# Optimization experiments

Hardware: AMD Instinct MI355X
Metric: run time of the kernel (lower is better)

Reference implementation:

```python
import jax, jax.numpy as jnp
import numpy as np

N = 8192   # nodes
D = 128    # uniform feature dim (arch = [128,128,128])
L = 2      # num_layers = len(arch)-1
EDGE_P = 0.01

def setup_inputs() -> dict:
    key = jax.random.key(0)
    ks = jax.random.split(key, 11)
    features = jax.random.normal(ks[0], (N, D), dtype=jnp.float32)
    # sparse symmetric adjacency with self-loops (diagonal forced True, as in forward)
    a = jax.random.uniform(ks[1], (N, N)) < EDGE_P
    mask = a | a.T | jnp.eye(N, dtype=bool)
    s = 1.0 / np.sqrt(D)
    def w(k):
        return (jax.random.normal(k, (L, D, D), dtype=jnp.float32) * s)
    def b(k):
        return jax.random.normal(k, (L, D), dtype=jnp.float32) * 0.01
    return {
        "features": features, "mask": mask,
        "Wq": w(ks[2]), "bq": b(ks[3]),
        "Wk": w(ks[4]), "bk": b(ks[5]),
        "Wv": w(ks[6]), "bv": b(ks[7]),
        "Wo": w(ks[8]), "bo": b(ks[9]),
    }

def reference(features, mask, Wq, bq, Wk, bk, Wv, bv, Wo, bo):
    h = features
    outputs = [h]
    for l in range(L):
        Q = h @ Wq[l] + bq[l]                      # [N, D]
        K = h @ Wk[l] + bk[l]
        V = h @ Wv[l] + bv[l]
        scores = (Q @ K.T) * (1.0 / jnp.sqrt(jnp.float32(K.shape[1])))  # [N, N]
        scores = jnp.where(mask, scores, -jnp.inf)
        attn = jax.nn.softmax(scores, axis=1)
        h = attn @ V                                # [N, D]
        h = h @ Wo[l] + bo[l]
        outputs.append(h)
    return tuple(outputs)
```

## Files before the change

kernel.cpp:

```cpp
#include <hip/hip_runtime.h>
#include <hip/hip_bf16.h>
#include <hip/hip_fp16.h>
#include <math.h>

#define N 8192
#define D 128
#define CAP 512

typedef _Float16 f16x2 __attribute__((ext_vector_type(2)));
typedef _Float16 f16x4 __attribute__((ext_vector_type(4)));
typedef _Float16 f16x8 __attribute__((ext_vector_type(8)));

__device__ __forceinline__ float dot2(f16x2 a, f16x2 b, float c) {
#if __has_builtin(__builtin_amdgcn_fdot2)
    return __builtin_amdgcn_fdot2(a, b, c, false);
#else
    return c + (float)a[0] * (float)b[0] + (float)a[1] * (float)b[1];
#endif
}

__device__ __forceinline__ float dot8(f16x8 a, f16x8 b, float c) {
    c = dot2(__builtin_shufflevector(a, a, 0, 1), __builtin_shufflevector(b, b, 0, 1), c);
    c = dot2(__builtin_shufflevector(a, a, 2, 3), __builtin_shufflevector(b, b, 2, 3), c);
    c = dot2(__builtin_shufflevector(a, a, 4, 5), __builtin_shufflevector(b, b, 4, 5), c);
    c = dot2(__builtin_shufflevector(a, a, 6, 7), __builtin_shufflevector(b, b, 6, 7), c);
    return c;
}

__global__ __launch_bounds__(256) void build_adj(const int* __restrict__ mask,
                                                 unsigned short* __restrict__ nbr,
                                                 int* __restrict__ deg) {
    const int i = blockIdx.x;
    __shared__ int cnt;
    if (threadIdx.x == 0) cnt = 0;
    __syncthreads();
    const int4* row = (const int4*)(mask + (size_t)i * N);
    for (int c = threadIdx.x; c < N / 4; c += 256) {
        int4 m4 = row[c];
        int base = 4 * c;
        if (m4.x) { int p = atomicAdd(&cnt, 1); if (p < CAP) nbr[(size_t)i * CAP + p] = (unsigned short)(base); }
        if (m4.y) { int p = atomicAdd(&cnt, 1); if (p < CAP) nbr[(size_t)i * CAP + p] = (unsigned short)(base + 1); }
        if (m4.z) { int p = atomicAdd(&cnt, 1); if (p < CAP) nbr[(size_t)i * CAP + p] = (unsigned short)(base + 2); }
        if (m4.w) { int p = atomicAdd(&cnt, 1); if (p < CAP) nbr[(size_t)i * CAP + p] = (unsigned short)(base + 3); }
    }
    __syncthreads();
    if (threadIdx.x == 0) deg[i] = (cnt > CAP) ? CAP : cnt;
}

__global__ __launch_bounds__(256) void qkv_gemm(const float* __restrict__ A,
                                                const float* __restrict__ Wq, const float* __restrict__ bq,
                                                const float* __restrict__ Wk, const float* __restrict__ bk,
                                                const float* __restrict__ Wv, const float* __restrict__ bv,
                                                __half* __restrict__ Qo, __half* __restrict__ Ko,
                                                __half* __restrict__ Vo,
                                                float* __restrict__ copy_out) {
    __shared__ float As[8][D];
    const int tid = threadIdx.x;
    const int r   = tid >> 5;
    const int jg  = tid & 31;
    const int i0  = blockIdx.x * 8;

    const float4 av = ((const float4*)(A + (size_t)i0 * D))[tid];
    ((float4*)&As[0][0])[tid] = av;
    ((float4*)(copy_out + (size_t)i0 * D))[tid] = av;
    __syncthreads();

    const float* Ws[3] = {Wq, Wk, Wv};
    const float* bs[3] = {bq, bk, bv};
    __half* Os[3] = {Qo, Ko, Vo};

    #pragma unroll
    for (int m = 0; m < 3; ++m) {
        float4 acc = *(const float4*)(bs[m] + 4 * jg);
        const float* W = Ws[m];
        #pragma unroll 8
        for (int k4 = 0; k4 < 32; ++k4) {
            const float4 a4 = *(const float4*)&As[r][4 * k4];
            const float* wb = W + (size_t)(4 * k4) * D + 4 * jg;
            const float4 w0 = *(const float4*)(wb);
            const float4 w1 = *(const float4*)(wb + D);
            const float4 w2 = *(const float4*)(wb + 2 * D);
            const float4 w3 = *(const float4*)(wb + 3 * D);
            acc.x += a4.x * w0.x + a4.y * w1.x + a4.z * w2.x + a4.w * w3.x;
            acc.y += a4.x * w0.y + a4.y * w1.y + a4.z * w2.y + a4.w * w3.y;
            acc.z += a4.x * w0.z + a4.y * w1.z + a4.z * w2.z + a4.w * w3.z;
            acc.w += a4.x * w0.w + a4.y * w1.w + a4.z * w2.w + a4.w * w3.w;
        }
        f16x4 h;
        h[0] = (_Float16)acc.x; h[1] = (_Float16)acc.y;
        h[2] = (_Float16)acc.z; h[3] = (_Float16)acc.w;
        *(f16x4*)(Os[m] + (size_t)(i0 + r) * D + 4 * jg) = h;
    }
}

__global__ __launch_bounds__(256) void gemmO_qkv(const float* __restrict__ Aattn,
                                                 const float* __restrict__ Wo, const float* __restrict__ bo,
                                                 float* __restrict__ Hout,
                                                 const float* __restrict__ Wq, const float* __restrict__ bq,
                                                 const float* __restrict__ Wk, const float* __restrict__ bk,
                                                 const float* __restrict__ Wv, const float* __restrict__ bv,
                                                 __half* __restrict__ Qo, __half* __restrict__ Ko,
                                                 __half* __restrict__ Vo) {
    __shared__ float As[8][D];
    __shared__ float Hs[8][D];
    const int tid = threadIdx.x;
    const int r   = tid >> 5;
    const int jg  = tid & 31;
    const int i0  = blockIdx.x * 8;

    ((float4*)&As[0][0])[tid] = ((const float4*)(Aattn + (size_t)i0 * D))[tid];
    __syncthreads();

    {
        float4 acc = *(const float4*)(bo + 4 * jg);
        #pragma unroll 8
        for (int k4 = 0; k4 < 32; ++k4) {
            const float4 a4 = *(const float4*)&As[r][4 * k4];
            const float* wb = Wo + (size_t)(4 * k4) * D + 4 * jg;
            const float4 w0 = *(const float4*)(wb);
            const float4 w1 = *(const float4*)(wb + D);
            const float4 w2 = *(const float4*)(wb + 2 * D);
            const float4 w3 = *(const float4*)(wb + 3 * D);
            acc.x += a4.x * w0.x + a4.y * w1.x + a4.z * w2.x + a4.w * w3.x;
            acc.y += a4.x * w0.y + a4.y * w1.y + a4.z * w2.y + a4.w * w3.y;
            acc.z += a4.x * w0.z + a4.y * w1.z + a4.z * w2.z + a4.w * w3.z;
            acc.w += a4.x * w0.w + a4.y * w1.w + a4.z * w2.w + a4.w * w3.w;
        }
        *(float4*)(Hout + (size_t)(i0 + r) * D + 4 * jg) = acc;
        *(float4*)&Hs[r][4 * jg] = acc;
    }
    __syncthreads();

    const float* Ws[3] = {Wq, Wk, Wv};
    const float* bs[3] = {bq, bk, bv};
    __half* Os[3] = {Qo, Ko, Vo};
    #pragma unroll
    for (int m = 0; m < 3; ++m) {
        float4 acc = *(const float4*)(bs[m] + 4 * jg);
        const float* W = Ws[m];
        #pragma unroll 8
        for (int k4 = 0; k4 < 32; ++k4) {
            const float4 a4 = *(const float4*)&Hs[r][4 * k4];
            const float* wb = W + (size_t)(4 * k4) * D + 4 * jg;
            const float4 w0 = *(const float4*)(wb);
            const float4 w1 = *(const float4*)(wb + D);
            const float4 w2 = *(const float4*)(wb + 2 * D);
            const float4 w3 = *(const float4*)(wb + 3 * D);
            acc.x += a4.x * w0.x + a4.y * w1.x + a4.z * w2.x + a4.w * w3.x;
            acc.y += a4.x * w0.y + a4.y * w1.y + a4.z * w2.y + a4.w * w3.y;
            acc.z += a4.x * w0.z + a4.y * w1.z + a4.z * w2.z + a4.w * w3.z;
            acc.w += a4.x * w0.w + a4.y * w1.w + a4.z * w2.w + a4.w * w3.w;
        }
        f16x4 h;
        h[0] = (_Float16)acc.x; h[1] = (_Float16)acc.y;
        h[2] = (_Float16)acc.z; h[3] = (_Float16)acc.w;
        *(f16x4*)(Os[m] + (size_t)(i0 + r) * D + 4 * jg) = h;
    }
}

__global__ __launch_bounds__(256) void gemm_bias(const float* __restrict__ A,
                                                 const float* __restrict__ W,
                                                 const float* __restrict__ bias,
                                                 float* __restrict__ C) {
    __shared__ float As[8][D];
    const int tid = threadIdx.x;
    const int r   = tid >> 5;
    const int jg  = tid & 31;
    const int i0  = blockIdx.x * 8;

    ((float4*)&As[0][0])[tid] = ((const float4*)(A + (size_t)i0 * D))[tid];
    __syncthreads();

    float4 acc = *(const float4*)(bias + 4 * jg);
    #pragma unroll 8
    for (int k4 = 0; k4 < 32; ++k4) {
        const float4 a4 = *(const float4*)&As[r][4 * k4];
        const float* wb = W + (size_t)(4 * k4) * D + 4 * jg;
        const float4 w0 = *(const float4*)(wb);
        const float4 w1 = *(const float4*)(wb + D);
        const float4 w2 = *(const float4*)(wb + 2 * D);
        const float4 w3 = *(const float4*)(wb + 3 * D);
        acc.x += a4.x * w0.x + a4.y * w1.x + a4.z * w2.x + a4.w * w3.x;
        acc.y += a4.x * w0.y + a4.y * w1.y + a4.z * w2.y + a4.w * w3.y;
        acc.z += a4.x * w0.z + a4.y * w1.z + a4.z * w2.z + a4.w * w3.z;
        acc.w += a4.x * w0.w + a4.y * w1.w + a4.z * w2.w + a4.w * w3.w;
    }
    *(float4*)(C + (size_t)(i0 + r) * D + 4 * jg) = acc;
}

__global__ __launch_bounds__(256) void attn_sparse(const __half* __restrict__ Q,
                                                   const __half* __restrict__ K,
                                                   const __half* __restrict__ V,
                                                   const unsigned short* __restrict__ nbr,
                                                   const int* __restrict__ deg,
                                                   float* __restrict__ Hout) {
    const int i    = blockIdx.x;
    const int tid  = threadIdx.x;
    const int wave = tid >> 6;
    const int lane = tid & 63;
    const int g    = lane >> 4;
    const int gl   = lane & 15;

    __shared__ float          s[CAP];
    __shared__ unsigned short jls[CAP];
    __shared__ float          red[16][D];
    __shared__ float          inv_sh;

    const int dg = min(deg[i], CAP);
    for (int e = tid; e < dg; e += 256) jls[e] = nbr[(size_t)i * CAP + e];
    const f16x8 qv = ((const f16x8*)(Q + (size_t)i * D))[gl];
    __syncthreads();

    const float scale = 0.088388347648318447f;

    for (int e = wave * 4 + g; e < dg; e += 16) {
        const f16x8 kv = ((const f16x8*)(K + (size_t)jls[e] * D))[gl];
        float dot = dot8(kv, qv, 0.f);
        dot += __shfl_xor(dot, 1);
        dot += __shfl_xor(dot, 2);
        dot += __shfl_xor(dot, 4);
        dot += __shfl_xor(dot, 8);
        if (gl == 0) s[e] = __expf(dot * scale);
    }
    __syncthreads();

    if (wave == 0) {
        float ls = 0.f;
        for (int e = lane; e < dg; e += 64) ls += s[e];
        #pragma unroll
        for (int off = 32; off > 0; off >>= 1)
            ls += __shfl_xor(ls, off);
        if (lane == 0) inv_sh = 1.0f / ls;
    }
    __syncthreads();

    const int slice = tid >> 4;
    float acc[8] = {0.f, 0.f, 0.f, 0.f, 0.f, 0.f, 0.f, 0.f};
    for (int e = slice; e < dg; e += 16) {
        const float p  = s[e];
        const f16x8 v8 = ((const f16x8*)(V + (size_t)jls[e] * D))[gl];
        #pragma unroll
        for (int k = 0; k < 8; ++k) acc[k] += p * (float)v8[k];
    }
    #pragma unroll
    for (int k = 0; k < 8; ++k) red[slice][8 * gl + k] = acc[k];
    __syncthreads();
    if (tid < D) {
        float sum = 0.f;
        #pragma unroll
        for (int sl = 0; sl < 16; ++sl) sum += red[sl][tid];
        Hout[(size_t)i * D + tid] = sum * inv_sh;
    }
}

extern "C" void kernel_launch(void* const* d_in, const int* in_sizes, int n_in,
                              void* d_out, int out_size, void* d_ws, size_t ws_size,
                              hipStream_t stream) {
    const float* features = (const float*)d_in[0];
    const int*   mask     = (const int*)d_in[1];
    const float* Wq = (const float*)d_in[2];
    const float* bq = (const float*)d_in[3];
    const float* Wk = (const float*)d_in[4];
    const float* bk = (const float*)d_in[5];
    const float* Wv = (const float*)d_in[6];
    const float* bv = (const float*)d_in[7];
    const float* Wo = (const float*)d_in[8];
    const float* bo = (const float*)d_in[9];
    float* out = (float*)d_out;

    char* base = (char*)d_ws;
    unsigned short* nbr = (unsigned short*)base;
    int*    deg  = (int*)(base + (size_t)N * CAP * 2);
    __half* Qb16 = (__half*)(base + (size_t)N * CAP * 2 + N * 4);
    __half* Kb16 = Qb16 + (size_t)N * D;
    __half* Vb16 = Kb16 + (size_t)N * D;
    float*  tmp  = (float*)(Vb16 + (size_t)N * D);

    build_adj<<<N, 256, 0, stream>>>(mask, nbr, deg);

    qkv_gemm<<<N / 8, 256, 0, stream>>>(features, Wq, bq, Wk, bk, Wv, bv,
                                        Qb16, Kb16, Vb16, out);
    attn_sparse<<<N, 256, 0, stream>>>(Qb16, Kb16, Vb16, nbr, deg, tmp);
    gemmO_qkv<<<N / 8, 256, 0, stream>>>(tmp, Wo, bo, out + (size_t)N * D,
                                         Wq + D * D, bq + D, Wk + D * D, bk + D,
                                         Wv + D * D, bv + D, Qb16, Kb16, Vb16);
    attn_sparse<<<N, 256, 0, stream>>>(Qb16, Kb16, Vb16, nbr, deg, tmp);
    gemm_bias<<<N / 8, 256, 0, stream>>>(tmp, Wo + D * D, bo + D,
                                         out + (size_t)2 * N * D);
}
```

Baseline: 610.3 us.

## Process one node per wave with fused single-pass softmax-weighted aggregation

The sparse attention kernel now assigns one destination node to each wavefront, so each block covers four nodes, instead of using a whole 256-thread block per node. The score, exp, denominator and V-accumulation steps are fused into one loop over neighbours, removing the shared score buffer, the separate reduction pass and two block barriers. Partial sums across the four 16-lane groups are combined with shuffles. It skips max subtraction, as the code before also did, and each wave still handles roughly 160 neighbours serially, so there is less parallelism per node.

```diff
diff --git a/kernel.cpp b/kernel.cpp
--- a/kernel.cpp
+++ b/kernel.cpp
@@ -194,62 +194,57 @@
                                                    const unsigned short* __restrict__ nbr,
                                                    const int* __restrict__ deg,
                                                    float* __restrict__ Hout) {
-    const int i    = blockIdx.x;
     const int tid  = threadIdx.x;
     const int wave = tid >> 6;
     const int lane = tid & 63;
     const int g    = lane >> 4;
     const int gl   = lane & 15;
-
-    __shared__ float          s[CAP];
-    __shared__ unsigned short jls[CAP];
-    __shared__ float          red[16][D];
-    __shared__ float          inv_sh;
+    const int i    = blockIdx.x * 4 + wave;
+
+    __shared__ unsigned short jls[4][CAP];
 
     const int dg = min(deg[i], CAP);
-    for (int e = tid; e < dg; e += 256) jls[e] = nbr[(size_t)i * CAP + e];
+    for (int e = lane; e < dg; e += 64)
+        jls[wave][e] = nbr[(size_t)i * CAP + e];
     const f16x8 qv = ((const f16x8*)(Q + (size_t)i * D))[gl];
     __syncthreads();
 
     const float scale = 0.088388347648318447f;
 
-    for (int e = wave * 4 + g; e < dg; e += 16) {
-        const f16x8 kv = ((const f16x8*)(K + (size_t)jls[e] * D))[gl];
+    float acc[8] = {0.f, 0.f, 0.f, 0.f, 0.f, 0.f, 0.f, 0.f};
+    float denom  = 0.f;
+
+    for (int e = g; e < dg; e += 4) {
+        const int j = jls[wave][e];
+        const f16x8 kv = ((const f16x8*)(K + (size_t)j * D))[gl];
         float dot = dot8(kv, qv, 0.f);
         dot += __shfl_xor(dot, 1);
         dot += __shfl_xor(dot, 2);
         dot += __shfl_xor(dot, 4);
         dot += __shfl_xor(dot, 8);
-        if (gl == 0) s[e] = __expf(dot * scale);
-    }
-    __syncthreads();
-
-    if (wave == 0) {
-        float ls = 0.f;
-        for (int e = lane; e < dg; e += 64) ls += s[e];
-        #pragma unroll
-        for (int off = 32; off > 0; off >>= 1)
-            ls += __shfl_xor(ls, off);
-        if (lane == 0) inv_sh = 1.0f / ls;
-    }
-    __syncthreads();
-
-    const int slice = tid >> 4;
-    float acc[8] = {0.f, 0.f, 0.f, 0.f, 0.f, 0.f, 0.f, 0.f};
-    for (int e = slice; e < dg; e += 16) {
-        const float p  = s[e];
-        const f16x8 v8 = ((const f16x8*)(V + (size_t)jls[e] * D))[gl];
+        const float p = __expf(dot * scale);
+        const f16x8 v8 = ((const f16x8*)(V + (size_t)j * D))[gl];
         #pragma unroll
         for (int k = 0; k < 8; ++k) acc[k] += p * (float)v8[k];
-    }
+        denom += p;
+    }
+
     #pragma unroll
-    for (int k = 0; k < 8; ++k) red[slice][8 * gl + k] = acc[k];
-    __syncthreads();
-    if (tid < D) {
-        float sum = 0.f;
-        #pragma unroll
-        for (int sl = 0; sl < 16; ++sl) sum += red[sl][tid];
-        Hout[(size_t)i * D + tid] = sum * inv_sh;
+    for (int k = 0; k < 8; ++k) {
+        acc[k] += __shfl_xor(acc[k], 16);
+        acc[k] += __shfl_xor(acc[k], 32);
+    }
+    denom += __shfl_xor(denom, 16);
+    denom += __shfl_xor(denom, 32);
+
+    if (g == 0) {
+        const float inv = 1.0f / denom;
+        float4 o0, o1;
+        o0.x = acc[0] * inv; o0.y = acc[1] * inv; o0.z = acc[2] * inv; o0.w = acc[3] * inv;
+        o1.x = acc[4] * inv; o1.y = acc[5] * inv; o1.z = acc[6] * inv; o1.w = acc[7] * inv;
+        float4* dst = (float4*)(Hout + (size_t)i * D + 8 * gl);
+        dst[0] = o0;
+        dst[1] = o1;
     }
 }
 
@@ -280,11 +275,11 @@
 
     qkv_gemm<<<N / 8, 256, 0, stream>>>(features, Wq, bq, Wk, bk, Wv, bv,
                                         Qb16, Kb16, Vb16, out);
-    attn_sparse<<<N, 256, 0, stream>>>(Qb16, Kb16, Vb16, nbr, deg, tmp);
+    attn_sparse<<<N / 4, 256, 0, stream>>>(Qb16, Kb16, Vb16, nbr, deg, tmp);
     gemmO_qkv<<<N / 8, 256, 0, stream>>>(tmp, Wo, bo, out + (size_t)N * D,
                                          Wq + D * D, bq + D, Wk + D * D, bk + D,
                                          Wv + D * D, bv + D, Qb16, Kb16, Vb16);
-    attn_sparse<<<N, 256, 0, stream>>>(Qb16, Kb16, Vb16, nbr, deg, tmp);
+    attn_sparse<<<N / 4, 256, 0, stream>>>(Qb16, Kb16, Vb16, nbr, deg, tmp);
     gemm_bias<<<N / 8, 256, 0, stream>>>(tmp, Wo + D * D, bo + D,
                                          out + (size_t)2 * N * D);
 }
```

Measured after the change: 577.1 us. -5.4%, faster.
